# Kernel optimization log

Measured on AMD Instinct MI355X. Metric: run time of the kernel, lower is better.

Reference implementation:

```python
import jax, jax.numpy as jnp
import numpy as np

N_ROWS = 200_000   # output dim (len(distances))
N_COLS = 200_000   # input dim
NNZ = N_ROWS * 64  # avg 64 neighbors per unitig


def setup_inputs() -> dict:
    key = jax.random.key(0)
    k1, k2, k3, k4, k5 = jax.random.split(key, 5)
    rows = jnp.sort(jax.random.randint(k1, (NNZ,), 0, N_ROWS))  # COO row ids, sorted
    cols = jax.random.randint(k2, (NNZ,), 0, N_COLS)            # COO col ids
    vals = jax.random.normal(k3, (NNZ,), dtype=jnp.float32)     # sparse weight values
    x = jax.random.normal(k4, (N_COLS, 1), dtype=jnp.float32)   # dense input column vector
    bias = jax.random.normal(k5, (N_ROWS,), dtype=jnp.float32)
    return {"vals": vals, "x": x, "bias": bias, "rows": rows, "cols": cols, "n_rows": N_ROWS}


def reference(vals, x, bias, rows, cols, n_rows):
    # y = sparse.mm(W, x).squeeze(1) + bias, W in COO form (rows, cols, vals)
    gathered = vals * x[cols, 0]                      # [nnz]
    y = jax.ops.segment_sum(gathered, rows, num_segments=n_rows,
                            indices_are_sorted=True)  # [n_rows]
    return y + bias
```

## Files before the change

### kernel.cpp

```cpp
#include <hip/hip_runtime.h>


constexpr int       CHUNK = 16;
constexpr int       BLOCK = 256;
constexpr long long SPAN  = (long long)BLOCK * CHUNK;
constexpr int       RMAX  = 6144;

typedef float vfloat4 __attribute__((ext_vector_type(4)));
typedef int   vint4   __attribute__((ext_vector_type(4)));

__global__ void init_y_bias(const float* __restrict__ bias,
                            float* __restrict__ y, int n) {
    int i = blockIdx.x * blockDim.x + threadIdx.x;
    if (i < n) y[i] = bias[i];
}

__device__ __forceinline__ void lds_add(float* p, float v) {
    __hip_atomic_fetch_add(p, v, __ATOMIC_RELAXED, __HIP_MEMORY_SCOPE_WORKGROUP);
}

__global__ __launch_bounds__(BLOCK) void spmv_coo_lds(
        const float* __restrict__ vals,
        const float* __restrict__ x,
        const int*   __restrict__ rows,
        const int*   __restrict__ cols,
        const float* __restrict__ bias,
        float*       __restrict__ y,
        long long nnz) {
    __shared__ float acc[RMAX];
    const int tid = threadIdx.x;
    const long long b0 = (long long)blockIdx.x * SPAN;
    if (b0 >= nnz) return;
    const long long bend = (b0 + SPAN < nnz) ? (b0 + SPAN) : nnz;

    const int r0    = rows[b0];
    const int rl    = rows[bend - 1];
    const int range = rl - r0 + 1;

    if (range <= RMAX) {
        for (int i = tid; i < range; i += BLOCK) acc[i] = 0.f;
        __syncthreads();

        const long long i0 = b0 + (long long)tid * CHUNK;
        if (i0 < bend) {
            if (i0 + CHUNK <= bend) {
                const vfloat4* v4 = reinterpret_cast<const vfloat4*>(vals + i0);
                const vint4*   r4 = reinterpret_cast<const vint4*>(rows + i0);
                const vint4*   c4 = reinterpret_cast<const vint4*>(cols + i0);
                float v[CHUNK]; int r[CHUNK]; int c[CHUNK];
                #pragma unroll
                for (int q = 0; q < CHUNK / 4; ++q) {
                    vfloat4 vv = __builtin_nontemporal_load(v4 + q);
                    vint4   rr = __builtin_nontemporal_load(r4 + q);
                    vint4   cc = __builtin_nontemporal_load(c4 + q);
                    #pragma unroll
                    for (int j = 0; j < 4; ++j) {
                        v[4*q+j] = vv[j];
                        r[4*q+j] = rr[j];
                        c[4*q+j] = cc[j];
                    }
                }
                float g[CHUNK];
                #pragma unroll
                for (int k = 0; k < CHUNK; ++k) g[k] = x[c[k]];

                int   cur = r[0];
                float sum = v[0] * g[0];
                #pragma unroll
                for (int k = 1; k < CHUNK; ++k) {
                    if (r[k] != cur) {
                        lds_add(&acc[cur - r0], sum);
                        cur = r[k];
                        sum = 0.f;
                    }
                    sum += v[k] * g[k];
                }
                lds_add(&acc[cur - r0], sum);
            } else {
                int   cur = rows[i0];
                float sum = 0.f;
                long long kend = (i0 + CHUNK < bend) ? (i0 + CHUNK) : bend;
                for (long long k = i0; k < kend; ++k) {
                    int rk = rows[k];
                    if (rk != cur) { lds_add(&acc[cur - r0], sum); sum = 0.f; cur = rk; }
                    sum += vals[k] * x[cols[k]];
                }
                lds_add(&acc[cur - r0], sum);
            }
        }
        __syncthreads();

        for (int i = tid; i < range; i += BLOCK) {
            int   r = r0 + i;
            float a = acc[i];
            if (r == r0 || r == rl) {
                if (a != 0.f) atomicAdd(&y[r], a);
            } else {
                y[r] = bias[r] + a;
            }
        }
    } else {
        const long long i0 = b0 + (long long)tid * CHUNK;
        if (i0 < bend) {
            int   cur = rows[i0];
            float sum = 0.f;
            long long kend = (i0 + CHUNK < bend) ? (i0 + CHUNK) : bend;
            for (long long k = i0; k < kend; ++k) {
                int rk = rows[k];
                if (rk != cur) { atomicAdd(&y[cur], sum); sum = 0.f; cur = rk; }
                sum += vals[k] * x[cols[k]];
            }
            atomicAdd(&y[cur], sum);
        }
    }
}

extern "C" void kernel_launch(void* const* d_in, const int* in_sizes, int n_in,
                              void* d_out, int out_size, void* d_ws, size_t ws_size,
                              hipStream_t stream) {
    const float* vals = (const float*)d_in[0];
    const float* x    = (const float*)d_in[1];
    const float* bias = (const float*)d_in[2];
    const int*   rows = (const int*)d_in[3];
    const int*   cols = (const int*)d_in[4];
    float* y = (float*)d_out;

    const long long nnz = in_sizes[0];
    const int n_rows    = in_sizes[2];

    {
        int threads = 256;
        int blocks  = (n_rows + threads - 1) / threads;
        init_y_bias<<<blocks, threads, 0, stream>>>(bias, y, n_rows);
    }

    {
        long long blocks = (nnz + SPAN - 1) / SPAN;
        spmv_coo_lds<<<(int)blocks, BLOCK, 0, stream>>>(
            vals, x, rows, cols, bias, y, nnz);
    }
}
```

Before: 218.1 us.

## Issue streaming loads before LDS zeroing and halve chunk size

Moves the vectorized nontemporal loads of vals, rows and cols ahead of the LDS accumulator zeroing, the row-range reads and the barrier, so global memory latency overlaps the setup work. CHUNK drops from 16 to 8 and RMAX from 6144 to 768. Blocks become smaller and more numerous, and the LDS footprint shrinks, which should allow more resident blocks per CU. The fallback path now reuses the preloaded registers and zeroes a fixed RMAX-sized buffer. In exchange, the smaller span raises the share of boundary rows handled with global atomics.

Result: faster. 208.9 us (-4.2%).

```diff
diff --git a/kernel.cpp b/kernel.cpp
--- a/kernel.cpp
+++ b/kernel.cpp
@@ -1,10 +1,10 @@
 #include <hip/hip_runtime.h>
 
 
-constexpr int       CHUNK = 16;
+constexpr int       CHUNK = 8;
 constexpr int       BLOCK = 256;
 constexpr long long SPAN  = (long long)BLOCK * CHUNK;
-constexpr int       RMAX  = 6144;
+constexpr int       RMAX  = 768;
 
 typedef float vfloat4 __attribute__((ext_vector_type(4)));
 typedef int   vint4   __attribute__((ext_vector_type(4)));
@@ -32,85 +32,100 @@
     const long long b0 = (long long)blockIdx.x * SPAN;
     if (b0 >= nnz) return;
     const long long bend = (b0 + SPAN < nnz) ? (b0 + SPAN) : nnz;
+    const bool full = (b0 + SPAN) <= nnz;
 
+    float v[CHUNK]; int r[CHUNK]; int c[CHUNK];
+    const long long i0 = b0 + (long long)tid * CHUNK;
+    if (full) {
+        const vfloat4* v4 = reinterpret_cast<const vfloat4*>(vals + i0);
+        const vint4*   r4 = reinterpret_cast<const vint4*>(rows + i0);
+        const vint4*   c4 = reinterpret_cast<const vint4*>(cols + i0);
+        #pragma unroll
+        for (int q = 0; q < CHUNK / 4; ++q) {
+            vfloat4 vv = __builtin_nontemporal_load(v4 + q);
+            vint4   rr = __builtin_nontemporal_load(r4 + q);
+            vint4   cc = __builtin_nontemporal_load(c4 + q);
+            #pragma unroll
+            for (int j = 0; j < 4; ++j) {
+                v[4*q+j] = vv[j];
+                r[4*q+j] = rr[j];
+                c[4*q+j] = cc[j];
+            }
+        }
+    }
+
+    #pragma unroll
+    for (int i = tid; i < RMAX; i += BLOCK) acc[i] = 0.f;
     const int r0    = rows[b0];
     const int rl    = rows[bend - 1];
     const int range = rl - r0 + 1;
+    __syncthreads();
 
     if (range <= RMAX) {
-        for (int i = tid; i < range; i += BLOCK) acc[i] = 0.f;
+        if (full) {
+            float g[CHUNK];
+            #pragma unroll
+            for (int k = 0; k < CHUNK; ++k) g[k] = x[c[k]];
+
+            int   cur = r[0];
+            float sum = v[0] * g[0];
+            #pragma unroll
+            for (int k = 1; k < CHUNK; ++k) {
+                if (r[k] != cur) {
+                    lds_add(&acc[cur - r0], sum);
+                    cur = r[k];
+                    sum = 0.f;
+                }
+                sum += v[k] * g[k];
+            }
+            lds_add(&acc[cur - r0], sum);
+        } else if (i0 < bend) {
+            int   cur = rows[i0];
+            float sum = 0.f;
+            long long kend = (i0 + CHUNK < bend) ? (i0 + CHUNK) : bend;
+            for (long long k = i0; k < kend; ++k) {
+                int rk = rows[k];
+                if (rk != cur) { lds_add(&acc[cur - r0], sum); sum = 0.f; cur = rk; }
+                sum += vals[k] * x[cols[k]];
+            }
+            lds_add(&acc[cur - r0], sum);
+        }
         __syncthreads();
 
-        const long long i0 = b0 + (long long)tid * CHUNK;
+        for (int i = tid; i < range; i += BLOCK) {
+            int   rr = r0 + i;
+            float a  = acc[i];
+            if (rr == r0 || rr == rl) {
+                if (a != 0.f) atomicAdd(&y[rr], a);
+            } else {
+                y[rr] = bias[rr] + a;
+            }
+        }
+    } else {
         if (i0 < bend) {
-            if (i0 + CHUNK <= bend) {
-                const vfloat4* v4 = reinterpret_cast<const vfloat4*>(vals + i0);
-                const vint4*   r4 = reinterpret_cast<const vint4*>(rows + i0);
-                const vint4*   c4 = reinterpret_cast<const vint4*>(cols + i0);
-                float v[CHUNK]; int r[CHUNK]; int c[CHUNK];
-                #pragma unroll
-                for (int q = 0; q < CHUNK / 4; ++q) {
-                    vfloat4 vv = __builtin_nontemporal_load(v4 + q);
-                    vint4   rr = __builtin_nontemporal_load(r4 + q);
-                    vint4   cc = __builtin_nontemporal_load(c4 + q);
-                    #pragma unroll
-                    for (int j = 0; j < 4; ++j) {
-                        v[4*q+j] = vv[j];
-                        r[4*q+j] = rr[j];
-                        c[4*q+j] = cc[j];
-                    }
-                }
+            if (full) {
                 float g[CHUNK];
                 #pragma unroll
                 for (int k = 0; k < CHUNK; ++k) g[k] = x[c[k]];
-
                 int   cur = r[0];
                 float sum = v[0] * g[0];
                 #pragma unroll
                 for (int k = 1; k < CHUNK; ++k) {
-                    if (r[k] != cur) {
-                        lds_add(&acc[cur - r0], sum);
-                        cur = r[k];
-                        sum = 0.f;
-                    }
+                    if (r[k] != cur) { atomicAdd(&y[cur], sum); sum = 0.f; cur = r[k]; }
                     sum += v[k] * g[k];
                 }
-                lds_add(&acc[cur - r0], sum);
+                atomicAdd(&y[cur], sum);
             } else {
                 int   cur = rows[i0];
                 float sum = 0.f;
                 long long kend = (i0 + CHUNK < bend) ? (i0 + CHUNK) : bend;
                 for (long long k = i0; k < kend; ++k) {
                     int rk = rows[k];
-                    if (rk != cur) { lds_add(&acc[cur - r0], sum); sum = 0.f; cur = rk; }
+                    if (rk != cur) { atomicAdd(&y[cur], sum); sum = 0.f; cur = rk; }
                     sum += vals[k] * x[cols[k]];
                 }
-                lds_add(&acc[cur - r0], sum);
+                atomicAdd(&y[cur], sum);
             }
-        }
-        __syncthreads();
-
-        for (int i = tid; i < range; i += BLOCK) {
-            int   r = r0 + i;
-            float a = acc[i];
-            if (r == r0 || r == rl) {
-                if (a != 0.f) atomicAdd(&y[r], a);
-            } else {
-                y[r] = bias[r] + a;
-            }
-        }
-    } else {
-        const long long i0 = b0 + (long long)tid * CHUNK;
-        if (i0 < bend) {
-            int   cur = rows[i0];
-            float sum = 0.f;
-            long long kend = (i0 + CHUNK < bend) ? (i0 + CHUNK) : bend;
-            for (long long k = i0; k < kend; ++k) {
-                int rk = rows[k];
-                if (rk != cur) { atomicAdd(&y[cur], sum); sum = 0.f; cur = rk; }
-                sum += vals[k] * x[cols[k]];
-            }
-            atomicAdd(&y[cur], sum);
         }
     }
 }
```
